# Performance work log

Measured on AMD Instinct MI355X. Metric: run time of the kernel, lower is better.

The kernel has to match this reference:

```python
import jax, jax.numpy as jnp
import numpy as np

C = 768      # atom_embedding_size
CP = 128     # atom_pair_embedding_size
H = 16       # num_head
D = C // H   # head dim = 48
HID = 2 * C  # SwiGLU hidden (n=2 per AF3 Algorithm 25)


def _ln(x, eps=1e-5):
    mu = jnp.mean(x, axis=-1, keepdims=True)
    var = jnp.var(x, axis=-1, keepdims=True)
    return (x - mu) * jax.lax.rsqrt(var + eps)


def ada_ln(a, s, sg, wg, bg, wsk):
    # AF3 Algorithm 26: a <- LN(a, no affine); s <- LN(s)*gamma (no bias);
    # a <- sigmoid(Linear(s)) * a + LinearNoBias(s)
    an = _ln(a)
    sn = _ln(s) * sg
    return jax.nn.sigmoid(sn @ wg + bg) * an + sn @ wsk


def setup_inputs() -> dict:
    key = jax.random.key(0)
    ks = jax.random.split(key, 24)
    B, N = 1, 1024
    w = lambda k, sh: jax.random.normal(k, sh, jnp.float32) * 0.02
    return {
        "a": jax.random.normal(ks[0], (B, N, C), jnp.float32),
        "s": jax.random.normal(ks[1], (B, N, C), jnp.float32),
        "pair_rep": jax.random.normal(ks[2], (B, N, N, CP), jnp.float32),
        "beta": jax.random.normal(ks[3], (B, N, N), jnp.float32),
        # AttentionPairBias params
        "sg1": jnp.ones((C,), jnp.float32),
        "wg1": w(ks[4], (C, C)), "bg1": jnp.zeros((C,), jnp.float32),
        "wsk1": w(ks[5], (C, C)),
        "wq": w(ks[6], (C, C)), "bq": jnp.zeros((C,), jnp.float32),
        "wk": w(ks[7], (C, C)), "wv": w(ks[8], (C, C)),
        "gp": jnp.ones((CP,), jnp.float32), "bp": jnp.zeros((CP,), jnp.float32),
        "wp": w(ks[9], (CP, H)),
        "wgate": w(ks[10], (C, C)),
        "wo": w(ks[11], (C, C)),
        "wso": w(ks[12], (C, C)), "bso": jnp.full((C,), -2.0, jnp.float32),
        # ConditionedTransitionBlock params
        "sg2": jnp.ones((C,), jnp.float32),
        "wg2": w(ks[13], (C, C)), "bg2": jnp.zeros((C,), jnp.float32),
        "wsk2": w(ks[14], (C, C)),
        "w1": w(ks[15], (C, HID)), "w2": w(ks[16], (C, HID)),
        "w3": w(ks[17], (HID, C)),
        "ws2": w(ks[18], (C, C)), "bs2": jnp.full((C,), -2.0, jnp.float32),
    }


def reference(a, s, pair_rep, beta, sg1, wg1, bg1, wsk1, wq, bq, wk, wv,
              gp, bp, wp, wgate, wo, wso, bso,
              sg2, wg2, bg2, wsk2, w1, w2, w3, ws2, bs2):
    B, N, _ = a.shape
    # ---- AttentionPairBias (AF3 Algorithm 24) ----
    an = ada_ln(a, s, sg1, wg1, bg1, wsk1)
    q = (an @ wq + bq).reshape(B, N, H, D)
    k = (an @ wk).reshape(B, N, H, D)
    v = (an @ wv).reshape(B, N, H, D)
    # pair bias: LN(pair) -> [B,N,N,H], plus scalar beta broadcast over heads
    z = (_ln(pair_rep) * gp + bp) @ wp                       # [B,N,N,H]
    bias = jnp.transpose(z, (0, 3, 1, 2)) + beta[:, None]    # [B,H,N,N]
    logits = jnp.einsum('bqhd,bkhd->bhqk', q, k) / np.float32(np.sqrt(D)) + bias
    attn = jax.nn.softmax(logits, axis=-1)
    o = jnp.einsum('bhqk,bkhd->bqhd', attn, v)               # [B,N,H,D]
    g = jax.nn.sigmoid(an @ wgate).reshape(B, N, H, D)
    att_out = (g * o).reshape(B, N, C) @ wo
    b_out = jax.nn.sigmoid(s @ wso + bso) * att_out
    # ---- ConditionedTransitionBlock (AF3 Algorithm 25, SwiGLU n=2) ----
    at = ada_ln(a, s, sg2, wg2, bg2, wsk2)
    hid = jax.nn.silu(at @ w1) * (at @ w2)
    t_out = jax.nn.sigmoid(s @ ws2 + bs2) * (hid @ w3)
    # ---- block: a = b + transition(a, s) ----
    return b_out + t_out
```

## Files before the change

kernel.cpp:

```cpp
#include <hip/hip_runtime.h>
#include <hip/hip_bf16.h>

typedef unsigned short u16;
typedef __attribute__((ext_vector_type(8))) short short8;
typedef __attribute__((ext_vector_type(4))) short short4v;
typedef __attribute__((ext_vector_type(4))) float f32x4;

__device__ __forceinline__ u16 f2bf(float f) {
  union { float f; unsigned int i; } v; v.f = f;
  unsigned int x = v.i;
  unsigned int r = x + 0x7fff + ((x >> 16) & 1);
  return (u16)(r >> 16);
}
__device__ __forceinline__ float bf2f(u16 u) {
  union { unsigned int i; float f; } v; v.i = ((unsigned int)u) << 16; return v.f;
}

struct TDesc { const float* src; u16* dst; int K; int N; };
struct TDescs { TDesc d[14]; };

__launch_bounds__(256)
__global__ void k_transpose(TDescs td) {
  TDesc t = td.d[blockIdx.z];
  int tk = blockIdx.y * 32, tn = blockIdx.x * 32;
  if (tk >= t.K || tn >= t.N) return;
  __shared__ u16 tile[32][33];
  int tx = threadIdx.x & 31, ty = threadIdx.x >> 5;
  for (int i = 0; i < 32; i += 8)
    tile[ty + i][tx] = f2bf(t.src[(long)(tk + ty + i) * t.N + tn + tx]);
  __syncthreads();
  for (int i = 0; i < 32; i += 8)
    t.dst[(long)(tn + ty + i) * t.K + tk + tx] = tile[tx][ty + i];
}

__launch_bounds__(256)
__global__ void k_layernorm(const float* __restrict__ a, const float* __restrict__ s,
                            const float* __restrict__ sg1, const float* __restrict__ sg2,
                            float* __restrict__ ln_a, u16* __restrict__ snb1,
                            u16* __restrict__ snb2, u16* __restrict__ sb) {
  const int row = blockIdx.x, tid = threadIdx.x;
  const float* ar = a + (long)row * 768;
  const float* sr = s + (long)row * 768;
  float av[3], sv[3];
  float sa = 0.f, sa2 = 0.f, ss = 0.f, ss2 = 0.f;
  for (int i = 0; i < 3; i++) {
    float x = ar[tid + i * 256]; av[i] = x; sa += x; sa2 += x * x;
    float y = sr[tid + i * 256]; sv[i] = y; ss += y; ss2 += y * y;
  }
  __shared__ float red[4][4];
  for (int off = 32; off > 0; off >>= 1) {
    sa += __shfl_down(sa, off); sa2 += __shfl_down(sa2, off);
    ss += __shfl_down(ss, off); ss2 += __shfl_down(ss2, off);
  }
  if ((tid & 63) == 0) { int w = tid >> 6; red[w][0] = sa; red[w][1] = sa2; red[w][2] = ss; red[w][3] = ss2; }
  __syncthreads();
  sa  = red[0][0] + red[1][0] + red[2][0] + red[3][0];
  sa2 = red[0][1] + red[1][1] + red[2][1] + red[3][1];
  ss  = red[0][2] + red[1][2] + red[2][2] + red[3][2];
  ss2 = red[0][3] + red[1][3] + red[2][3] + red[3][3];
  const float n1 = 1.f / 768.f;
  float mua = sa * n1, vara = sa2 * n1 - mua * mua;
  float mus = ss * n1, vars = ss2 * n1 - mus * mus;
  float ra = rsqrtf(vara + 1e-5f), rs = rsqrtf(vars + 1e-5f);
  for (int i = 0; i < 3; i++) {
    int c = tid + i * 256;
    long idx = (long)row * 768 + c;
    ln_a[idx] = (av[i] - mua) * ra;
    float lns = (sv[i] - mus) * rs;
    snb1[idx] = f2bf(lns * sg1[c]);
    snb2[idx] = f2bf(lns * sg2[c]);
    sb[idx]   = f2bf(sv[i]);
  }
}

__launch_bounds__(256)
__global__ void k_gemm_bt(const u16* __restrict__ A, const u16* __restrict__ BT,
                          float* __restrict__ C, int M, int N, int K) {
  __shared__ u16 As[64][40];
  __shared__ u16 Bs[64][40];
  const int tid = threadIdx.x;
  const int n0 = blockIdx.x * 64, m0 = blockIdx.y * 64;
  const int wave = tid >> 6, lane = tid & 63;
  const int wr = (wave >> 1) * 32, wc = (wave & 1) * 32;
  const int lrow = lane & 15, quad = lane >> 4;
  const int ldr = tid >> 2, ldk = (tid & 3) * 8;
  f32x4 acc00 = {0,0,0,0}, acc01 = {0,0,0,0}, acc10 = {0,0,0,0}, acc11 = {0,0,0,0};
  const u16* Ap = A + (long)(m0 + ldr) * K + ldk;
  const u16* Bp = BT + (long)(n0 + ldr) * K + ldk;
  for (int k0 = 0; k0 < K; k0 += 32) {
    __syncthreads();
    *(short8*)&As[ldr][ldk] = *(const short8*)(Ap + k0);
    *(short8*)&Bs[ldr][ldk] = *(const short8*)(Bp + k0);
    __syncthreads();
    short8 a0 = *(const short8*)&As[wr + lrow][quad * 8];
    short8 a1 = *(const short8*)&As[wr + 16 + lrow][quad * 8];
    short8 b0 = *(const short8*)&Bs[wc + lrow][quad * 8];
    short8 b1 = *(const short8*)&Bs[wc + 16 + lrow][quad * 8];
    acc00 = __builtin_amdgcn_mfma_f32_16x16x32_bf16(a0, b0, acc00, 0, 0, 0);
    acc01 = __builtin_amdgcn_mfma_f32_16x16x32_bf16(a0, b1, acc01, 0, 0, 0);
    acc10 = __builtin_amdgcn_mfma_f32_16x16x32_bf16(a1, b0, acc10, 0, 0, 0);
    acc11 = __builtin_amdgcn_mfma_f32_16x16x32_bf16(a1, b1, acc11, 0, 0, 0);
  }
  const int row = m0 + wr + quad * 4;
  const int col = n0 + wc + lrow;
  for (int r = 0; r < 4; r++) {
    C[(long)(row + r) * N + col]           = acc00[r];
    C[(long)(row + r) * N + col + 16]      = acc01[r];
    C[(long)(row + r + 16) * N + col]      = acc10[r];
    C[(long)(row + r + 16) * N + col + 16] = acc11[r];
  }
}

__launch_bounds__(256)
__global__ void k_adaln2(const float* __restrict__ g1, const float* __restrict__ g2,
                         const float* __restrict__ ln_a, const float* __restrict__ bg1,
                         const float* __restrict__ bg2, u16* __restrict__ an1,
                         u16* __restrict__ at2) {
  int i = blockIdx.x * 256 + threadIdx.x;
  int c = i % 768; long m = i / 768;
  float lna = ln_a[i];
  float x1 = g1[m * 1536 + c], y1 = g1[m * 1536 + 768 + c];
  float x2 = g2[m * 1536 + c], y2 = g2[m * 1536 + 768 + c];
  float s1 = 1.f / (1.f + __expf(-(x1 + bg1[c])));
  float s2 = 1.f / (1.f + __expf(-(x2 + bg2[c])));
  an1[i] = f2bf(s1 * lna + y1);
  at2[i] = f2bf(s2 * lna + y2);
}

__launch_bounds__(256)
__global__ void k_pairbias(const float* __restrict__ pair, const float* __restrict__ beta,
                           const float* __restrict__ gp, const float* __restrict__ bp,
                           const float* __restrict__ wp, u16* __restrict__ biasb) {
  __shared__ u16 Xs[64][136];
  __shared__ u16 Wb[16][136];
  __shared__ float Mu[64], Rs[64];
  __shared__ float AB[2][16];
  const int tid = threadIdx.x;
  const long base = (long)blockIdx.x * 64;
  for (int i = tid; i < 2048; i += 256) {
    int c = i >> 4, h = i & 15;
    Wb[h][c] = f2bf(gp[c] * wp[i]);
  }
  if (tid < 32) {
    int h = tid & 15;
    float acc = 0.f;
    if (tid < 16) { for (int c = 0; c < 128; c++) acc += gp[c] * wp[c * 16 + h]; }
    else          { for (int c = 0; c < 128; c++) acc += bp[c] * wp[c * 16 + h]; }
    AB[tid >> 4][h] = acc;
  }
  const int e = tid >> 2, r = tid & 3;
  const float* px = pair + (base + e) * 128 + r * 4;
  float sum = 0.f, sq = 0.f;
  for (int p = 0; p < 8; p++) {
    f32x4 x = *(const f32x4*)(px + p * 16);
    sum += x[0] + x[1] + x[2] + x[3];
    sq  += x[0]*x[0] + x[1]*x[1] + x[2]*x[2] + x[3]*x[3];
    short4v pk;
    pk[0] = (short)f2bf(x[0]); pk[1] = (short)f2bf(x[1]);
    pk[2] = (short)f2bf(x[2]); pk[3] = (short)f2bf(x[3]);
    *(short4v*)&Xs[e][r * 4 + p * 16] = pk;
  }
  sum += __shfl_xor(sum, 1); sum += __shfl_xor(sum, 2);
  sq  += __shfl_xor(sq, 1);  sq  += __shfl_xor(sq, 2);
  if (r == 0) {
    float mu = sum * (1.f / 128.f);
    float var = sq * (1.f / 128.f) - mu * mu;
    Mu[e] = mu; Rs[e] = rsqrtf(var + 1e-5f);
  }
  __syncthreads();
  const int wave = tid >> 6, lane = tid & 63;
  const int m = lane & 15, quad = lane >> 4;
  const int erow = wave * 16;
  f32x4 acc = {0, 0, 0, 0};
  for (int k0 = 0; k0 < 128; k0 += 32) {
    short8 af = *(const short8*)&Xs[erow + m][k0 + quad * 8];
    short8 bf = *(const short8*)&Wb[m][k0 + quad * 8];
    acc = __builtin_amdgcn_mfma_f32_16x16x32_bf16(af, bf, acc, 0, 0, 0);
  }
  const int h = lane & 15;
  const float Ahv = AB[0][h], Bhv = AB[1][h];
  const int e0 = erow + quad * 4;
  short4v outp;
  for (int rr = 0; rr < 4; rr++) {
    int ee = e0 + rr;
    float bt = beta[base + ee];
    float val = Rs[ee] * acc[rr] - Rs[ee] * Mu[ee] * Ahv + Bhv + bt;
    outp[rr] = (short)f2bf(val);
  }
  *(short4v*)&biasb[((long)h << 20) + base + e0] = outp;
}

__launch_bounds__(256)
__global__ void k_attention(const float* __restrict__ qkvg, const float* __restrict__ bq,
                            const u16* __restrict__ biasb, float* __restrict__ o_out) {
  const int h = blockIdx.y;
  const int q0 = blockIdx.x * 64;
  __shared__ u16 Ks[2][64][72];
  __shared__ u16 Vt[2][48][72];
  __shared__ u16 Ps[4][16][72];
  const int tid = threadIdx.x;
  const int w = tid >> 6, lane = tid & 63;
  const int lr = lane & 15, quad = lane >> 4;
  const float scale = 0.14433756729740643f;

  for (int i = tid; i < 2 * 64 * 16; i += 256) {
    int b = i >> 10, rr = (i >> 4) & 63, c = 48 + (i & 15);
    Ks[b][rr][c] = 0;
  }

  short8 qf0, qf1;
  {
    const int qrow = q0 + w * 16 + lr;
    const float* qp = qkvg + (long)qrow * 3072 + h * 48;
    const float* bqp = bq + h * 48;
    const int d0 = quad * 8;
#pragma unroll
    for (int i = 0; i < 8; i++)
      qf0[i] = (short)f2bf((qp[d0 + i] + bqp[d0 + i]) * scale);
    if (quad < 2) {
      const int d1 = 32 + quad * 8;
#pragma unroll
      for (int i = 0; i < 8; i++)
        qf1[i] = (short)f2bf((qp[d1 + i] + bqp[d1 + i]) * scale);
    } else {
#pragma unroll
      for (int i = 0; i < 8; i++) qf1[i] = 0;
    }
  }

  int sr[3], sc[3];
#pragma unroll
  for (int j = 0; j < 3; j++) { int i = tid + j * 256; sr[j] = i / 12; sc[j] = i % 12; }
  f32x4 kx[3], vx[3];

  float m[4], l[4];
#pragma unroll
  for (int r = 0; r < 4; r++) { m[r] = -1e30f; l[r] = 0.f; }
  f32x4 o0 = {0,0,0,0}, o1 = {0,0,0,0}, o2 = {0,0,0,0};

#pragma unroll
  for (int j = 0; j < 3; j++) {
    const float* p = qkvg + (long)sr[j] * 3072 + h * 48 + sc[j] * 4;
    kx[j] = *(const f32x4*)(p + 768);
    vx[j] = *(const f32x4*)(p + 1536);
  }
#pragma unroll
  for (int j = 0; j < 3; j++) {
    short4v pk;
#pragma unroll
    for (int e = 0; e < 4; e++) pk[e] = (short)f2bf(kx[j][e]);
    *(short4v*)&Ks[0][sr[j]][sc[j] * 4] = pk;
#pragma unroll
    for (int e = 0; e < 4; e++) Vt[0][sc[j] * 4 + e][sr[j]] = f2bf(vx[j][e]);
  }

  const long bbase = ((long)h << 20) + (long)(q0 + w * 16 + quad * 4) * 1024 + lr;
  int cur = 0;

  for (int t = 0; t < 16; t++) {
    __syncthreads();
    if (t < 15) {
      const int kt = (t + 1) * 64;
#pragma unroll
      for (int j = 0; j < 3; j++) {
        const float* p = qkvg + (long)(kt + sr[j]) * 3072 + h * 48 + sc[j] * 4;
        kx[j] = *(const f32x4*)(p + 768);
        vx[j] = *(const f32x4*)(p + 1536);
      }
    }
    u16 bw[16];
    const u16* bpt = biasb + bbase + t * 64;
#pragma unroll
    for (int j = 0; j < 4; j++)
#pragma unroll
      for (int r = 0; r < 4; r++)
        bw[j * 4 + r] = bpt[r * 1024 + j * 16];
    f32x4 sv[4];
#pragma unroll
    for (int j = 0; j < 4; j++) {
      short8 kb0 = *(const short8*)&Ks[cur][j * 16 + lr][quad * 8];
      short8 kb1 = *(const short8*)&Ks[cur][j * 16 + lr][32 + quad * 8];
      f32x4 z = {0,0,0,0};
      z = __builtin_amdgcn_mfma_f32_16x16x32_bf16(qf0, kb0, z, 0, 0, 0);
      z = __builtin_amdgcn_mfma_f32_16x16x32_bf16(qf1, kb1, z, 0, 0, 0);
      sv[j] = z;
    }
#pragma unroll
    for (int j = 0; j < 4; j++)
#pragma unroll
      for (int r = 0; r < 4; r++)
        sv[j][r] += bf2f(bw[j * 4 + r]);
    float alpha[4];
#pragma unroll
    for (int r = 0; r < 4; r++) {
      float tmax = fmaxf(fmaxf(sv[0][r], sv[1][r]), fmaxf(sv[2][r], sv[3][r]));
      tmax = fmaxf(tmax, __shfl_xor(tmax, 1));
      tmax = fmaxf(tmax, __shfl_xor(tmax, 2));
      tmax = fmaxf(tmax, __shfl_xor(tmax, 4));
      tmax = fmaxf(tmax, __shfl_xor(tmax, 8));
      float mn = fmaxf(m[r], tmax);
      alpha[r] = __expf(m[r] - mn);
      m[r] = mn;
      float ps = 0.f;
#pragma unroll
      for (int j = 0; j < 4; j++) { float p = __expf(sv[j][r] - mn); sv[j][r] = p; ps += p; }
      ps += __shfl_xor(ps, 1); ps += __shfl_xor(ps, 2);
      ps += __shfl_xor(ps, 4); ps += __shfl_xor(ps, 8);
      l[r] = l[r] * alpha[r] + ps;
    }
    f32x4 al = {alpha[0], alpha[1], alpha[2], alpha[3]};
    o0 *= al; o1 *= al; o2 *= al;
#pragma unroll
    for (int j = 0; j < 4; j++)
#pragma unroll
      for (int r = 0; r < 4; r++)
        Ps[w][quad * 4 + r][j * 16 + lr] = f2bf(sv[j][r]);
#pragma unroll
    for (int kk = 0; kk < 2; kk++) {
      short8 pa  = *(const short8*)&Ps[w][lr][kk * 32 + quad * 8];
      short8 vb0 = *(const short8*)&Vt[cur][lr][kk * 32 + quad * 8];
      short8 vb1 = *(const short8*)&Vt[cur][16 + lr][kk * 32 + quad * 8];
      short8 vb2 = *(const short8*)&Vt[cur][32 + lr][kk * 32 + quad * 8];
      o0 = __builtin_amdgcn_mfma_f32_16x16x32_bf16(pa, vb0, o0, 0, 0, 0);
      o1 = __builtin_amdgcn_mfma_f32_16x16x32_bf16(pa, vb1, o1, 0, 0, 0);
      o2 = __builtin_amdgcn_mfma_f32_16x16x32_bf16(pa, vb2, o2, 0, 0, 0);
    }
    if (t < 15) {
      const int nb = cur ^ 1;
#pragma unroll
      for (int j = 0; j < 3; j++) {
        short4v pk;
#pragma unroll
        for (int e = 0; e < 4; e++) pk[e] = (short)f2bf(kx[j][e]);
        *(short4v*)&Ks[nb][sr[j]][sc[j] * 4] = pk;
#pragma unroll
        for (int e = 0; e < 4; e++) Vt[nb][sc[j] * 4 + e][sr[j]] = f2bf(vx[j][e]);
      }
    }
    cur ^= 1;
  }

  f32x4 linv = {1.f / l[0], 1.f / l[1], 1.f / l[2], 1.f / l[3]};
  o0 *= linv; o1 *= linv; o2 *= linv;
  const long ob = (long)(q0 + w * 16 + quad * 4) * 768 + h * 48 + lr;
#pragma unroll
  for (int r = 0; r < 4; r++) {
    o_out[ob + (long)r * 768]      = o0[r];
    o_out[ob + (long)r * 768 + 16] = o1[r];
    o_out[ob + (long)r * 768 + 32] = o2[r];
  }
}

__launch_bounds__(256)
__global__ void k_gateo(const float* __restrict__ qkvg, const float* __restrict__ o,
                        u16* __restrict__ go) {
  int i = blockIdx.x * 256 + threadIdx.x;
  int c = i % 768; long m = i / 768;
  float g = qkvg[m * 3072 + 2304 + c];
  float sg = 1.f / (1.f + __expf(-g));
  go[i] = f2bf(sg * o[i]);
}

__launch_bounds__(256)
__global__ void k_swiglu(const float* __restrict__ h12, u16* __restrict__ hid) {
  int i = blockIdx.x * 256 + threadIdx.x;
  int c = i % 1536; long m = i / 1536;
  float x = h12[m * 3072 + c], y = h12[m * 3072 + 1536 + c];
  float si = x / (1.f + __expf(-x));
  hid[i] = f2bf(si * y);
}

__launch_bounds__(256)
__global__ void k_final(const float* __restrict__ sgr, const float* __restrict__ att_out,
                        const float* __restrict__ t3, const float* __restrict__ bso,
                        const float* __restrict__ bs2, float* __restrict__ out) {
  int i = blockIdx.x * 256 + threadIdx.x;
  int c = i % 768; long m = i / 768;
  float g1 = 1.f / (1.f + __expf(-(sgr[m * 1536 + c] + bso[c])));
  float g2 = 1.f / (1.f + __expf(-(sgr[m * 1536 + 768 + c] + bs2[c])));
  out[i] = g1 * att_out[i] + g2 * t3[i];
}

extern "C" void kernel_launch(void* const* d_in, const int* in_sizes, int n_in,
                              void* d_out, int out_size, void* d_ws, size_t ws_size,
                              hipStream_t stream) {
  const float* a    = (const float*)d_in[0];
  const float* s    = (const float*)d_in[1];
  const float* pair = (const float*)d_in[2];
  const float* beta = (const float*)d_in[3];
  const float* sg1  = (const float*)d_in[4];
  const float* wg1  = (const float*)d_in[5];
  const float* bg1  = (const float*)d_in[6];
  const float* wsk1 = (const float*)d_in[7];
  const float* wq   = (const float*)d_in[8];
  const float* bq   = (const float*)d_in[9];
  const float* wk   = (const float*)d_in[10];
  const float* wv   = (const float*)d_in[11];
  const float* gp   = (const float*)d_in[12];
  const float* bp   = (const float*)d_in[13];
  const float* wp   = (const float*)d_in[14];
  const float* wgate= (const float*)d_in[15];
  const float* wo   = (const float*)d_in[16];
  const float* wso  = (const float*)d_in[17];
  const float* bso  = (const float*)d_in[18];
  const float* sg2  = (const float*)d_in[19];
  const float* wg2  = (const float*)d_in[20];
  const float* bg2  = (const float*)d_in[21];
  const float* wsk2 = (const float*)d_in[22];
  const float* w1   = (const float*)d_in[23];
  const float* w2   = (const float*)d_in[24];
  const float* w3   = (const float*)d_in[25];
  const float* ws2  = (const float*)d_in[26];
  const float* bs2  = (const float*)d_in[27];

  char* ws = (char*)d_ws;
  const long E = 589824;
  u16* WT     = (u16*)ws;
  u16* wgsk1T = WT;
  u16* wgsk2T = WT + 2 * E;
  u16* wqkvgT = WT + 4 * E;
  u16* wsos2T = WT + 8 * E;
  u16* woT    = WT + 10 * E;
  u16* w12T   = WT + 11 * E;
  u16* w3T    = WT + 15 * E;
  size_t off = 17 * E * 2;

  float* ln_a  = (float*)(ws + off); off += 786432 * 4;
  u16*   snb1  = (u16*)(ws + off);   off += 786432 * 2;
  u16*   snb2  = (u16*)(ws + off);   off += 786432 * 2;
  u16*   sb    = (u16*)(ws + off);   off += 786432 * 2;
  u16*   an1   = (u16*)(ws + off);   off += 786432 * 2;
  u16*   at2   = (u16*)(ws + off);   off += 786432 * 2;
  float* out12 = (float*)(ws + off); off += 1572864 * 4;
  float* out34 = (float*)(ws + off); off += 1572864 * 4;
  float* qkvg  = (float*)(ws + off); off += 3145728 * 4;
  float* h12   = qkvg;
  float* o_buf = (float*)(ws + off); off += 786432 * 4;
  u16*   go    = (u16*)(ws + off);   off += 786432 * 2;
  float* att_o = (float*)(ws + off); off += 786432 * 4;
  float* sgr   = (float*)(ws + off); off += 1572864 * 4;
  u16*   hid   = (u16*)(ws + off);   off += 1572864 * 2;
  float* t3    = (float*)(ws + off); off += 786432 * 4;
  u16*   biasb = (u16*)(ws + off);   off += (long)16 * 1024 * 1024 * 2;

  TDescs td;
  td.d[0]  = {wg1,   wgsk1T,         768, 768};
  td.d[1]  = {wsk1,  wgsk1T + E,     768, 768};
  td.d[2]  = {wg2,   wgsk2T,         768, 768};
  td.d[3]  = {wsk2,  wgsk2T + E,     768, 768};
  td.d[4]  = {wq,    wqkvgT,         768, 768};
  td.d[5]  = {wk,    wqkvgT + E,     768, 768};
  td.d[6]  = {wv,    wqkvgT + 2 * E, 768, 768};
  td.d[7]  = {wgate, wqkvgT + 3 * E, 768, 768};
  td.d[8]  = {wso,   wsos2T,         768, 768};
  td.d[9]  = {ws2,   wsos2T + E,     768, 768};
  td.d[10] = {wo,    woT,            768, 768};
  td.d[11] = {w1,    w12T,           768, 1536};
  td.d[12] = {w2,    w12T + 2 * E,   768, 1536};
  td.d[13] = {w3,    w3T,            1536, 768};

  k_transpose<<<dim3(48, 48, 14), 256, 0, stream>>>(td);
  k_layernorm<<<1024, 256, 0, stream>>>(a, s, sg1, sg2, ln_a, snb1, snb2, sb);
  k_gemm_bt<<<dim3(24, 16), 256, 0, stream>>>(snb1, wgsk1T, out12, 1024, 1536, 768);
  k_gemm_bt<<<dim3(24, 16), 256, 0, stream>>>(snb2, wgsk2T, out34, 1024, 1536, 768);
  k_adaln2<<<3072, 256, 0, stream>>>(out12, out34, ln_a, bg1, bg2, an1, at2);
  k_gemm_bt<<<dim3(48, 16), 256, 0, stream>>>(an1, wqkvgT, qkvg, 1024, 3072, 768);
  k_pairbias<<<16384, 256, 0, stream>>>(pair, beta, gp, bp, wp, biasb);
  k_attention<<<dim3(16, 16), 256, 0, stream>>>(qkvg, bq, biasb, o_buf);
  k_gateo<<<3072, 256, 0, stream>>>(qkvg, o_buf, go);
  k_gemm_bt<<<dim3(12, 16), 256, 0, stream>>>(go, woT, att_o, 1024, 768, 768);
  k_gemm_bt<<<dim3(24, 16), 256, 0, stream>>>(sb, wsos2T, sgr, 1024, 1536, 768);
  k_gemm_bt<<<dim3(48, 16), 256, 0, stream>>>(at2, w12T, h12, 1024, 3072, 768);
  k_swiglu<<<6144, 256, 0, stream>>>(h12, hid);
  k_gemm_bt<<<dim3(12, 16), 256, 0, stream>>>(hid, w3T, t3, 1024, 768, 1536);
  k_final<<<3072, 256, 0, stream>>>(sgr, att_o, t3, bso, bs2, (float*)d_out);
}
```

Baseline: 964.6 us.

## Double-buffer GEMM K-tiles and fuse sigmoid gating into attention epilogue

The bf16 GEMM now stages 64-wide K tiles in double-buffered shared memory and prefetches the next tile into registers while the MFMAs run on the current one, which halves the barrier count per K. Separately, the attention kernel now applies the sigmoid gate and 1/l normalization itself and writes bf16 output directly, removing the k_gateo launch and the fp32 o buffer round trip. The costs are more shared memory per GEMM block and the assumption that K is a multiple of 64, which holds for all calls here.

```diff
diff --git a/kernel.cpp b/kernel.cpp
--- a/kernel.cpp
+++ b/kernel.cpp
@@ -76,30 +76,49 @@
 __launch_bounds__(256)
 __global__ void k_gemm_bt(const u16* __restrict__ A, const u16* __restrict__ BT,
                           float* __restrict__ C, int M, int N, int K) {
-  __shared__ u16 As[64][40];
-  __shared__ u16 Bs[64][40];
+  __shared__ u16 As[2][64][72];
+  __shared__ u16 Bs[2][64][72];
   const int tid = threadIdx.x;
   const int n0 = blockIdx.x * 64, m0 = blockIdx.y * 64;
   const int wave = tid >> 6, lane = tid & 63;
   const int wr = (wave >> 1) * 32, wc = (wave & 1) * 32;
   const int lrow = lane & 15, quad = lane >> 4;
-  const int ldr = tid >> 2, ldk = (tid & 3) * 8;
+  const int r0 = tid >> 3, ck = (tid & 7) * 8;
   f32x4 acc00 = {0,0,0,0}, acc01 = {0,0,0,0}, acc10 = {0,0,0,0}, acc11 = {0,0,0,0};
-  const u16* Ap = A + (long)(m0 + ldr) * K + ldk;
-  const u16* Bp = BT + (long)(n0 + ldr) * K + ldk;
-  for (int k0 = 0; k0 < K; k0 += 32) {
+  const u16* Ap0 = A + (long)(m0 + r0) * K + ck;
+  const u16* Ap1 = A + (long)(m0 + r0 + 32) * K + ck;
+  const u16* Bp0 = BT + (long)(n0 + r0) * K + ck;
+  const u16* Bp1 = BT + (long)(n0 + r0 + 32) * K + ck;
+  short8 a0v = *(const short8*)(Ap0), a1v = *(const short8*)(Ap1);
+  short8 b0v = *(const short8*)(Bp0), b1v = *(const short8*)(Bp1);
+  *(short8*)&As[0][r0][ck] = a0v; *(short8*)&As[0][r0 + 32][ck] = a1v;
+  *(short8*)&Bs[0][r0][ck] = b0v; *(short8*)&Bs[0][r0 + 32][ck] = b1v;
+  const int T = K >> 6;
+  int cur = 0;
+  for (int t = 0; t < T; t++) {
     __syncthreads();
-    *(short8*)&As[ldr][ldk] = *(const short8*)(Ap + k0);
-    *(short8*)&Bs[ldr][ldk] = *(const short8*)(Bp + k0);
-    __syncthreads();
-    short8 a0 = *(const short8*)&As[wr + lrow][quad * 8];
-    short8 a1 = *(const short8*)&As[wr + 16 + lrow][quad * 8];
-    short8 b0 = *(const short8*)&Bs[wc + lrow][quad * 8];
-    short8 b1 = *(const short8*)&Bs[wc + 16 + lrow][quad * 8];
-    acc00 = __builtin_amdgcn_mfma_f32_16x16x32_bf16(a0, b0, acc00, 0, 0, 0);
-    acc01 = __builtin_amdgcn_mfma_f32_16x16x32_bf16(a0, b1, acc01, 0, 0, 0);
-    acc10 = __builtin_amdgcn_mfma_f32_16x16x32_bf16(a1, b0, acc10, 0, 0, 0);
-    acc11 = __builtin_amdgcn_mfma_f32_16x16x32_bf16(a1, b1, acc11, 0, 0, 0);
+    if (t + 1 < T) {
+      const int ko = (t + 1) * 64;
+      a0v = *(const short8*)(Ap0 + ko); a1v = *(const short8*)(Ap1 + ko);
+      b0v = *(const short8*)(Bp0 + ko); b1v = *(const short8*)(Bp1 + ko);
+    }
+#pragma unroll
+    for (int kk = 0; kk < 2; kk++) {
+      short8 af0 = *(const short8*)&As[cur][wr + lrow][kk * 32 + quad * 8];
+      short8 af1 = *(const short8*)&As[cur][wr + 16 + lrow][kk * 32 + quad * 8];
+      short8 bf0 = *(const short8*)&Bs[cur][wc + lrow][kk * 32 + quad * 8];
+      short8 bf1 = *(const short8*)&Bs[cur][wc + 16 + lrow][kk * 32 + quad * 8];
+      acc00 = __builtin_amdgcn_mfma_f32_16x16x32_bf16(af0, bf0, acc00, 0, 0, 0);
+      acc01 = __builtin_amdgcn_mfma_f32_16x16x32_bf16(af0, bf1, acc01, 0, 0, 0);
+      acc10 = __builtin_amdgcn_mfma_f32_16x16x32_bf16(af1, bf0, acc10, 0, 0, 0);
+      acc11 = __builtin_amdgcn_mfma_f32_16x16x32_bf16(af1, bf1, acc11, 0, 0, 0);
+    }
+    if (t + 1 < T) {
+      const int nb = cur ^ 1;
+      *(short8*)&As[nb][r0][ck] = a0v; *(short8*)&As[nb][r0 + 32][ck] = a1v;
+      *(short8*)&Bs[nb][r0][ck] = b0v; *(short8*)&Bs[nb][r0 + 32][ck] = b1v;
+    }
+    cur ^= 1;
   }
   const int row = m0 + wr + quad * 4;
   const int col = n0 + wc + lrow;
@@ -192,7 +211,7 @@
 
 __launch_bounds__(256)
 __global__ void k_attention(const float* __restrict__ qkvg, const float* __restrict__ bq,
-                            const u16* __restrict__ biasb, float* __restrict__ o_out) {
+                            const u16* __restrict__ biasb, u16* __restrict__ go) {
   const int h = blockIdx.y;
   const int q0 = blockIdx.x * 64;
   __shared__ u16 Ks[2][64][72];
@@ -340,25 +359,21 @@
     cur ^= 1;
   }
 
-  f32x4 linv = {1.f / l[0], 1.f / l[1], 1.f / l[2], 1.f / l[3]};
-  o0 *= linv; o1 *= linv; o2 *= linv;
-  const long ob = (long)(q0 + w * 16 + quad * 4) * 768 + h * 48 + lr;
+  const int qrow0 = q0 + w * 16 + quad * 4;
+  const int colb = h * 48 + lr;
 #pragma unroll
   for (int r = 0; r < 4; r++) {
-    o_out[ob + (long)r * 768]      = o0[r];
-    o_out[ob + (long)r * 768 + 16] = o1[r];
-    o_out[ob + (long)r * 768 + 32] = o2[r];
-  }
-}
-
-__launch_bounds__(256)
-__global__ void k_gateo(const float* __restrict__ qkvg, const float* __restrict__ o,
-                        u16* __restrict__ go) {
-  int i = blockIdx.x * 256 + threadIdx.x;
-  int c = i % 768; long m = i / 768;
-  float g = qkvg[m * 3072 + 2304 + c];
-  float sg = 1.f / (1.f + __expf(-g));
-  go[i] = f2bf(sg * o[i]);
+    const int row = qrow0 + r;
+    const float inv = 1.f / l[r];
+    const float* gpt = qkvg + (long)row * 3072 + 2304 + colb;
+    float g0 = 1.f / (1.f + __expf(-gpt[0]));
+    float g1 = 1.f / (1.f + __expf(-gpt[16]));
+    float g2 = 1.f / (1.f + __expf(-gpt[32]));
+    u16* gop = go + (long)row * 768 + colb;
+    gop[0]  = f2bf(g0 * o0[r] * inv);
+    gop[16] = f2bf(g1 * o1[r] * inv);
+    gop[32] = f2bf(g2 * o2[r] * inv);
+  }
 }
 
 __launch_bounds__(256)
@@ -435,7 +450,6 @@
   float* out34 = (float*)(ws + off); off += 1572864 * 4;
   float* qkvg  = (float*)(ws + off); off += 3145728 * 4;
   float* h12   = qkvg;
-  float* o_buf = (float*)(ws + off); off += 786432 * 4;
   u16*   go    = (u16*)(ws + off);   off += 786432 * 2;
   float* att_o = (float*)(ws + off); off += 786432 * 4;
   float* sgr   = (float*)(ws + off); off += 1572864 * 4;
@@ -466,8 +480,7 @@
   k_adaln2<<<3072, 256, 0, stream>>>(out12, out34, ln_a, bg1, bg2, an1, at2);
   k_gemm_bt<<<dim3(48, 16), 256, 0, stream>>>(an1, wqkvgT, qkvg, 1024, 3072, 768);
   k_pairbias<<<16384, 256, 0, stream>>>(pair, beta, gp, bp, wp, biasb);
-  k_attention<<<dim3(16, 16), 256, 0, stream>>>(qkvg, bq, biasb, o_buf);
-  k_gateo<<<3072, 256, 0, stream>>>(qkvg, o_buf, go);
+  k_attention<<<dim3(16, 16), 256, 0, stream>>>(qkvg, bq, biasb, go);
   k_gemm_bt<<<dim3(12, 16), 256, 0, stream>>>(go, woT, att_o, 1024, 768, 768);
   k_gemm_bt<<<dim3(24, 16), 256, 0, stream>>>(sb, wsos2T, sgr, 1024, 1536, 768);
   k_gemm_bt<<<dim3(48, 16), 256, 0, stream>>>(at2, w12T, h12, 1024, 3072, 768);
```

New measurement: 926.2 us. 4.0% less time.
